# Performance work log

Measured on AMD Instinct MI355X. Metric: run time of the kernel, lower is better.

The kernel has to match this reference:

```python
import jax, jax.numpy as jnp
import numpy as np
from jax import lax

DIM, D_STATE, D_CONV, EXPAND = 96, 16, 4, 2
D_INNER = EXPAND * DIM          # 192
DT_RANK = (DIM + 15) // 16      # 6
B_, T_, H_, W_ = 2, 8, 32, 32   # L = T*H*W = 8192 tokens


def setup_inputs() -> dict:
    key = jax.random.key(0)
    ks = jax.random.split(key, 16)
    f = jnp.float32
    rn = lambda k, shape, s=0.02: jax.random.normal(k, shape, dtype=f) * s
    # S4D-real init for A_log, as in mamba_ssm
    A_init = jnp.log(jnp.tile(jnp.arange(1, D_STATE + 1, dtype=f), (D_INNER, 1)))
    return dict(
        x=jax.random.normal(ks[0], (B_, DIM, T_, H_, W_), dtype=f),
        ln_gamma=1.0 + rn(ks[1], (DIM,)),
        ln_beta=rn(ks[2], (DIM,)),
        in_proj_w=rn(ks[3], (2 * D_INNER, DIM)),
        conv_w=rn(ks[4], (D_INNER, 1, D_CONV), 0.1),
        conv_b=rn(ks[5], (D_INNER,)),
        x_proj_w=rn(ks[6], (DT_RANK + 2 * D_STATE, D_INNER)),
        dt_proj_w=rn(ks[7], (D_INNER, DT_RANK), 0.1),
        dt_proj_b=rn(ks[8], (D_INNER,)) + 0.5,
        A_log=A_init,
        D=jnp.ones((D_INNER,), f),
        conv_w_b=rn(ks[9], (D_INNER, 1, D_CONV), 0.1),
        conv_b_b=rn(ks[10], (D_INNER,)),
        x_proj_w_b=rn(ks[11], (DT_RANK + 2 * D_STATE, D_INNER)),
        dt_proj_w_b=rn(ks[12], (D_INNER, DT_RANK), 0.1),
        dt_proj_b_b=rn(ks[13], (D_INNER,)) + 0.5,
        A_log_b=A_init,
        D_b=jnp.ones((D_INNER,), f),
        out_proj_w=rn(ks[14], (DIM, D_INNER)),
    )


def serpentine(x):
    # continues_scan: reverse W on odd H rows so flattened (T,H,W) ordering is a
    # continuous path through the volume. Involutive => also rev_continues_scan.
    return x.at[..., 1::2, :].set(jnp.flip(x[..., 1::2, :], axis=-1))


def layer_norm(x, g, b, eps=1e-5):
    mu = jnp.mean(x, -1, keepdims=True)
    var = jnp.var(x, -1, keepdims=True)
    return (x - mu) * lax.rsqrt(var + eps) * g + b


def mamba_dir(x_in, z, conv_w, conv_b, x_proj_w, dt_proj_w, dt_proj_b, A_log, D):
    # x_in, z: (B, L, d_inner). One directional selective-scan branch.
    xc = lax.conv_general_dilated(
        x_in.swapaxes(1, 2), conv_w, (1,), [(D_CONV - 1, 0)],
        feature_group_count=D_INNER, dimension_numbers=('NCH', 'OIH', 'NCH'))
    xc = jax.nn.silu(xc + conv_b[None, :, None]).swapaxes(1, 2)  # (B,L,d_inner)
    dbl = jnp.einsum('bld,ed->ble', xc, x_proj_w)                # (B,L,dt_rank+2N)
    dt = jax.nn.softplus(
        jnp.einsum('blr,dr->bld', dbl[..., :DT_RANK], dt_proj_w) + dt_proj_b)
    Bm = dbl[..., DT_RANK:DT_RANK + D_STATE]                     # (B,L,N)
    Cm = dbl[..., DT_RANK + D_STATE:]                            # (B,L,N)
    A = -jnp.exp(A_log)                                          # (d_inner,N)

    def step(h, inp):
        dt_t, x_t, B_t, C_t = inp                                # (B,d),(B,d),(B,N),(B,N)
        h = jnp.exp(dt_t[..., None] * A) * h + (dt_t * x_t)[..., None] * B_t[:, None, :]
        return h, jnp.einsum('bdn,bn->bd', h, C_t)

    h0 = jnp.zeros((x_in.shape[0], D_INNER, D_STATE), x_in.dtype)
    xs = (dt.swapaxes(0, 1), xc.swapaxes(0, 1), Bm.swapaxes(0, 1), Cm.swapaxes(0, 1))
    _, ys = lax.scan(step, h0, xs)                               # (L,B,d_inner)
    y = ys.swapaxes(0, 1) + D * xc
    return y * jax.nn.silu(z)


def reference(x, ln_gamma, ln_beta, in_proj_w, conv_w, conv_b, x_proj_w,
              dt_proj_w, dt_proj_b, A_log, D, conv_w_b, conv_b_b, x_proj_w_b,
              dt_proj_w_b, dt_proj_b_b, A_log_b, D_b, out_proj_w):
    B, C, T, H, W = x.shape
    xs = serpentine(x)
    x_flat = xs.reshape(B, C, T * H * W).swapaxes(1, 2)          # (B,L,dim)
    xn = layer_norm(x_flat, ln_gamma, ln_beta)
    xz = jnp.einsum('bld,ed->ble', xn, in_proj_w)                # (B,L,2*d_inner)
    x_in, z = jnp.split(xz, 2, axis=-1)
    y_f = mamba_dir(x_in, z, conv_w, conv_b, x_proj_w, dt_proj_w,
                    dt_proj_b, A_log, D)
    y_b = jnp.flip(
        mamba_dir(jnp.flip(x_in, 1), jnp.flip(z, 1), conv_w_b, conv_b_b,
                  x_proj_w_b, dt_proj_w_b, dt_proj_b_b, A_log_b, D_b), 1)
    out = jnp.einsum('bld,ed->ble', y_f + y_b, out_proj_w)       # (B,L,dim)
    out = out.swapaxes(1, 2).reshape(B, C, T, H, W)
    return serpentine(out)
```

## Files before the change

### kernel.cpp

```cpp
#include <hip/hip_runtime.h>
#include <math.h>

#define LSEQ 8192
#define TS   32
#define NST  8

template<int CTRL>
__device__ __forceinline__ float dpp_add(float x) {
  const int y = __builtin_amdgcn_update_dpp(0, __float_as_int(x), CTRL, 0xF, 0xF, true);
  return x + __int_as_float(y);
}
__device__ __forceinline__ float red16(float x) {
  x = dpp_add<0xB1>(x);
  x = dpp_add<0x4E>(x);
  x = dpp_add<0x128>(x);
  x = dpp_add<0x124>(x);
  return x;
}

__global__ __launch_bounds__(256) void k0_wt(const float* __restrict__ xw_f,
    const float* __restrict__ xw_b, const float* __restrict__ in_w,
    const float* __restrict__ ow, float* __restrict__ xwT,
    float* __restrict__ inwT, float* __restrict__ owT) {
  const int step = gridDim.x * 256;
  const int t0 = blockIdx.x * 256 + threadIdx.x;
  for (int idx = t0; idx < 2 * 192 * 40; idx += step) {
    const int dir = idx / (192 * 40), rem = idx - dir * 192 * 40;
    const int k = rem / 40, r = rem - k * 40;
    const float* w = dir ? xw_b : xw_f;
    xwT[idx] = (r < 38) ? w[r * 192 + k] : 0.f;
  }
  for (int idx = t0; idx < 96 * 384; idx += step) {
    const int k = idx / 384, e = idx - k * 384;
    inwT[idx] = in_w[e * 96 + k];
  }
  for (int idx = t0; idx < 192 * 96; idx += step) {
    const int k = idx / 96, e = idx - k * 96;
    owT[idx] = ow[e * 192 + k];
  }
}

__global__ __launch_bounds__(256) void k1_serp_ln(const float* __restrict__ x,
    const float* __restrict__ gam, const float* __restrict__ bet,
    float* __restrict__ xnT) {
  const int b  = blockIdx.x >> 7;
  const int l0 = (blockIdx.x & 127) << 6;
  __shared__ float xs[96][65];
  __shared__ float mu[64], rs[64];
  const int tid = threadIdx.x;
  for (int idx = tid; idx < 96 * 64; idx += 256) {
    const int c = idx >> 6, l = idx & 63;
    const int lg = l0 + l;
    const int hh = (lg >> 5) & 31, w = lg & 31;
    const int lsrc = (hh & 1) ? (lg + 31 - 2 * w) : lg;
    xs[c][l] = x[(b * 96 + c) * LSEQ + lsrc];
  }
  __syncthreads();
  {
    const int l = tid >> 2, k = tid & 3;
    float s = 0.f, s2 = 0.f;
    for (int c = k; c < 96; c += 4) { const float v = xs[c][l]; s += v; s2 += v * v; }
    s  += __shfl_xor(s, 1);  s  += __shfl_xor(s, 2);
    s2 += __shfl_xor(s2, 1); s2 += __shfl_xor(s2, 2);
    if (k == 0) {
      const float m = s * (1.f / 96.f);
      const float var = s2 * (1.f / 96.f) - m * m;
      mu[l] = m; rs[l] = rsqrtf(var + 1e-5f);
    }
  }
  __syncthreads();
  for (int idx = tid; idx < 96 * 64; idx += 256) {
    const int c = idx >> 6, l = idx & 63;
    xnT[c * 16384 + (b << 13) + l0 + l] =
        (xs[c][l] - mu[l]) * rs[l] * gam[c] + bet[c];
  }
}

__global__ __launch_bounds__(256) void k2_inproj(const float* __restrict__ xnT,
    const float* __restrict__ inwT, float* __restrict__ xz) {
  const int m0 = blockIdx.x << 6;
  const int e0 = blockIdx.y << 6;
  __shared__ float As[96][67];
  __shared__ float Ws[96][67];
  const int tid = threadIdx.x;
  for (int idx = tid; idx < 96 * 64; idx += 256) {
    const int k = idx >> 6, r = idx & 63;
    As[k][r] = xnT[(size_t)k * 16384 + m0 + r];
    Ws[k][r] = inwT[k * 384 + e0 + r];
  }
  __syncthreads();
  const int tx = tid & 15, ty = tid >> 4;
  const int la = tx << 2, ea = ty << 2;
  float acc[4][4] = {};
  for (int k = 0; k < 96; ++k) {
    float av[4], bv[4];
#pragma unroll
    for (int i = 0; i < 4; ++i) av[i] = As[k][la + i];
#pragma unroll
    for (int j = 0; j < 4; ++j) bv[j] = Ws[k][ea + j];
#pragma unroll
    for (int j = 0; j < 4; ++j)
#pragma unroll
      for (int i = 0; i < 4; ++i) acc[j][i] = fmaf(bv[j], av[i], acc[j][i]);
  }
  const int b = m0 >> 13, l0 = m0 & (LSEQ - 1);
  const bool dos = (e0 >= 192);
#pragma unroll
  for (int j = 0; j < 4; ++j) {
    const int e = e0 + ea + j;
    float4 v;
    v.x = acc[j][0]; v.y = acc[j][1]; v.z = acc[j][2]; v.w = acc[j][3];
    if (dos) {
      v.x = v.x / (1.f + __expf(-v.x)); v.y = v.y / (1.f + __expf(-v.y));
      v.z = v.z / (1.f + __expf(-v.z)); v.w = v.w / (1.f + __expf(-v.w));
    }
    *(float4*)(&xz[((size_t)b * 384 + e) * LSEQ + l0 + la]) = v;
  }
}

__global__ __launch_bounds__(256) void k3a_conv(const float* __restrict__ xz,
    const float* __restrict__ cw_f, const float* __restrict__ cb_f,
    const float* __restrict__ cw_b, const float* __restrict__ cb_b,
    float* __restrict__ xc) {
  const int l = (blockIdx.x << 8) + threadIdx.x;
  const int d = blockIdx.y, b = blockIdx.z;
  const float* xin = xz + ((size_t)b * 384 + d) * LSEQ;
  float xv[7];
#pragma unroll
  for (int j = -3; j <= 3; ++j) {
    const int ls = l + j;
    xv[j + 3] = ((unsigned)ls < LSEQ) ? xin[ls] : 0.f;
  }
  float af = cb_f[d], ab = cb_b[d];
#pragma unroll
  for (int j = 0; j < 4; ++j) {
    af = fmaf(cw_f[d * 4 + j], xv[j], af);
    ab = fmaf(cw_b[d * 4 + j], xv[6 - j], ab);
  }
  xc[((size_t)(b)       * 192 + d) * LSEQ + l] = af / (1.f + __expf(-af));
  xc[((size_t)(2 + b)   * 192 + d) * LSEQ + l] = ab / (1.f + __expf(-ab));
}

__global__ __launch_bounds__(256, 2) void k3b_xproj(const float* __restrict__ xc,
    const float* __restrict__ xwT,
    const float* __restrict__ dtw_f, const float* __restrict__ dtb_f,
    const float* __restrict__ dtw_b, const float* __restrict__ dtb_b,
    float* __restrict__ dt, float* __restrict__ Bo, float* __restrict__ Co) {
  __shared__ float part[4][38][65];
  __shared__ float sdbl[6][65];
  const int dirb = blockIdx.y, dir = dirb >> 1;
  const int tid = threadIdx.x;
  const int lane = tid & 63, w = tid >> 6;
  const int l0 = blockIdx.x << 6;
  const float* pc = xc + (size_t)dirb * 192 * LSEQ + l0 + lane;
  const float* wt = xwT + dir * 192 * 40;
  float acc[38];
#pragma unroll
  for (int r = 0; r < 38; ++r) acc[r] = 0.f;
  const int kbase = w * 48;
#pragma unroll 2
  for (int kk = 0; kk < 48; ++kk) {
    const int k = kbase + kk;
    const float v = pc[(size_t)k * LSEQ];
    const float* wk = wt + k * 40;
#pragma unroll
    for (int r = 0; r < 38; ++r) acc[r] = fmaf(wk[r], v, acc[r]);
  }
#pragma unroll
  for (int r = 0; r < 38; ++r) part[w][r][lane] = acc[r];
  __syncthreads();
  {
    const int lq = tid >> 2, g = tid & 3;
    float vB[4], vC[4];
#pragma unroll
    for (int i = 0; i < 4; ++i) {
      const int rB = 6 + 4 * g + i, rC = 22 + 4 * g + i;
      float sB = 0.f, sC = 0.f;
#pragma unroll
      for (int ww = 0; ww < 4; ++ww) {
        sB += part[ww][rB][lq];
        sC += part[ww][rC][lq];
      }
      vB[i] = sB; vC[i] = sC;
    }
    const size_t off = ((size_t)dirb * LSEQ + l0 + lq) * 16 + 4 * g;
    *(float4*)&Bo[off] = make_float4(vB[0], vB[1], vB[2], vB[3]);
    *(float4*)&Co[off] = make_float4(vC[0], vC[1], vC[2], vC[3]);
  }
  for (int r = w; r < 6; r += 4) {
    float s = 0.f;
#pragma unroll
    for (int ww = 0; ww < 4; ++ww) s += part[ww][r][lane];
    sdbl[r][lane] = s;
  }
  __syncthreads();
  const float* dw = dir ? dtw_b : dtw_f;
  const float* db = dir ? dtb_b : dtb_f;
  const float v0 = sdbl[0][lane], v1 = sdbl[1][lane], v2 = sdbl[2][lane],
              v3 = sdbl[3][lane], v4 = sdbl[4][lane], v5 = sdbl[5][lane];
  float* pdt = dt + (size_t)dirb * 192 * LSEQ + l0 + lane;
#pragma unroll 2
  for (int i = 0; i < 48; ++i) {
    const int d = w * 48 + i;
    float s = db[d];
    s = fmaf(dw[d * 6 + 0], v0, s);
    s = fmaf(dw[d * 6 + 1], v1, s);
    s = fmaf(dw[d * 6 + 2], v2, s);
    s = fmaf(dw[d * 6 + 3], v3, s);
    s = fmaf(dw[d * 6 + 4], v4, s);
    s = fmaf(dw[d * 6 + 5], v5, s);
    pdt[(size_t)d * LSEQ] = (s > 20.f) ? s : __logf(1.f + __expf(s));
  }
}

template<int DIR>
__device__ __forceinline__ void scanA_body(
    float2 (*sdt)[16][34], float (*sb)[TS][16],
    const float* __restrict__ dtg, const float* __restrict__ xcg,
    const float* __restrict__ pB, const float* __restrict__ Al,
    float* __restrict__ Pb, float* __restrict__ Hb, int b, int c, int dg) {
  const int tid = threadIdx.x;
  const int dl = tid >> 4, n = tid & 15;
  const int dirb = DIR * 2 + b;
  const int d = (dg << 4) + dl;
  const float Adn = -__expf(Al[d * 16 + n]);
  const float* dtp = dtg + ((size_t)(dirb * 192) + d) * LSEQ;
  const float* xcp = xcg + ((size_t)(dirb * 192) + d) * LSEQ;
  const int c0 = c << 8;
  const int tl2 = (tid & 15) * 2;
  const int br = tid >> 3, bcc = (tid & 7) * 2;
  {
    const int t0 = c0 + (DIR ? (NST - 1) : 0) * TS;
    const float2 a  = *(const float2*)&dtp[t0 + tl2];
    const float2 xu = *(const float2*)&xcp[t0 + tl2];
    const float2 rb = *(const float2*)&pB[(size_t)(t0 + br) * 16 + bcc];
    float4 pk; pk.x = a.x; pk.y = a.x * xu.x; pk.z = a.y; pk.w = a.y * xu.y;
    *(float4*)&sdt[0][dl][tl2] = pk;
    *(float2*)&sb[0][br][bcc] = rb;
  }
  __syncthreads();
  float h = 0.f, dts = 0.f;
  int buf = 0;
  for (int i = 0; i < NST; ++i) {
    const int s = DIR ? (NST - 1 - i) : i;
    float2 a = make_float2(0.f, 0.f), xu = make_float2(0.f, 0.f);
    float2 rb = make_float2(0.f, 0.f);
    if (i + 1 < NST) {
      const int t0n = c0 + (DIR ? (s - 1) : (s + 1)) * TS;
      a   = *(const float2*)&dtp[t0n + tl2];
      xu  = *(const float2*)&xcp[t0n + tl2];
      rb  = *(const float2*)&pB[(size_t)(t0n + br) * 16 + bcc];
    }
#pragma unroll
    for (int tt = 0; tt < TS; ++tt) {
      const int t = DIR ? (TS - 1 - tt) : tt;
      const float2 xv = sdt[buf][dl][t];
      const float Bn = sb[buf][t][n];
      const float av = __expf(xv.x * Adn);
      h = fmaf(av, h, xv.y * Bn);
      dts += xv.x;
    }
    if (i + 1 < NST) {
      float4 pk; pk.x = a.x; pk.y = a.x * xu.x; pk.z = a.y; pk.w = a.y * xu.y;
      *(float4*)&sdt[buf ^ 1][dl][tl2] = pk;
      *(float2*)&sb[buf ^ 1][br][bcc] = rb;
    }
    __syncthreads();
    buf ^= 1;
  }
  const int o = ((dirb * 32 + c) * 192 + d) * 16 + n;
  Pb[o] = __expf(dts * Adn);
  Hb[o] = h;
}

__global__ __launch_bounds__(256) void k4_scanA(const float* __restrict__ dtg,
    const float* __restrict__ xcg, const float* __restrict__ Bo,
    const float* __restrict__ Al_f, const float* __restrict__ Al_b,
    float* __restrict__ Pb, float* __restrict__ Hb) {
  __shared__ float2 sdt[2][16][34];
  __shared__ float sb[2][TS][16];
  const int b = blockIdx.y, c = blockIdx.x & 31, dg = blockIdx.x >> 5;
  const float* pB0 = Bo + (size_t)(0 * 2 + b) * LSEQ * 16;
  const float* pB1 = Bo + (size_t)(1 * 2 + b) * LSEQ * 16;
  if (blockIdx.z == 0) scanA_body<0>(sdt, sb, dtg, xcg, pB0, Al_f, Pb, Hb, b, c, dg);
  else                 scanA_body<1>(sdt, sb, dtg, xcg, pB1, Al_b, Pb, Hb, b, c, dg);
}

__global__ __launch_bounds__(256) void k5_scanB(const float* __restrict__ Pb,
    const float* __restrict__ Hb, float* __restrict__ H0) {
  const int g = blockIdx.x * 256 + threadIdx.x;
  const int dirb = g / 3072, dn = g - dirb * 3072;
  const int dir = dirb >> 1;
  const int base = dirb * (32 * 3072) + dn;
  float h = 0.f;
  if (dir == 0) {
    for (int c = 0; c < 32; ++c) {
      const int o = base + c * 3072;
      H0[o] = h;
      h = fmaf(Pb[o], h, Hb[o]);
    }
  } else {
    for (int c = 31; c >= 0; --c) {
      const int o = base + c * 3072;
      H0[o] = h;
      h = fmaf(Pb[o], h, Hb[o]);
    }
  }
}

template<int DIR>
__device__ __forceinline__ void scanC_body(
    float2 (*sdt)[16][34], float2 (*sbc)[TS][16],
    const float* __restrict__ dtg, const float* __restrict__ xcg,
    const float* __restrict__ pB, const float* __restrict__ pC,
    const float* __restrict__ xz,
    const float* __restrict__ Al, const float* __restrict__ Dv_,
    const float* __restrict__ H0, float* __restrict__ yout,
    int b, int c, int dg) {
  const int tid = threadIdx.x;
  const int dl = tid >> 4, n = tid & 15;
  const int dirb = DIR * 2 + b;
  const int d = (dg << 4) + dl;
  const float Adn = -__expf(Al[d * 16 + n]);
  const float Dv = Dv_[d];
  const float* dtp = dtg + ((size_t)(dirb * 192) + d) * LSEQ;
  const float* xcp = xcg + ((size_t)(dirb * 192) + d) * LSEQ;
  const float* psp = xz + ((size_t)(b * 384) + 192 + d) * LSEQ;
  float* py = yout + ((size_t)(b * 192) + d) * LSEQ;
  const int o = ((dirb * 32 + c) * 192 + d) * 16 + n;
  const int c0 = c << 8;
  const int tl2 = (tid & 15) * 2;
  const int br = tid >> 3, bcc = (tid & 7) * 2;
  float h = H0[o];
  const int t00 = c0 + (DIR ? (NST - 1) : 0) * TS;
  {
    const float2 a  = *(const float2*)&dtp[t00 + tl2];
    const float2 xu = *(const float2*)&xcp[t00 + tl2];
    const float2 b2 = *(const float2*)&pB[(size_t)(t00 + br) * 16 + bcc];
    const float2 c2 = *(const float2*)&pC[(size_t)(t00 + br) * 16 + bcc];
    float4 pk; pk.x = a.x; pk.y = a.x * xu.x; pk.z = a.y; pk.w = a.y * xu.y;
    *(float4*)&sdt[0][dl][tl2] = pk;
    *(float4*)&sbc[0][br][bcc] = make_float4(b2.x, c2.x, b2.y, c2.y);
  }
  float cxa = xcp[t00 + n], cxb = xcp[t00 + 16 + n];
  float cspa = psp[t00 + n], cspb = psp[t00 + 16 + n];
  __syncthreads();
  int buf = 0;
  for (int i = 0; i < NST; ++i) {
    const int s = DIR ? (NST - 1 - i) : i;
    const int t0 = c0 + s * TS;
    float2 a = make_float2(0.f, 0.f), xu = make_float2(0.f, 0.f);
    float2 b2 = make_float2(0.f, 0.f), c2 = make_float2(0.f, 0.f);
    float nxa = 0.f, nxb = 0.f, nspa = 0.f, nspb = 0.f;
    if (i + 1 < NST) {
      const int t0n = c0 + (DIR ? (s - 1) : (s + 1)) * TS;
      a   = *(const float2*)&dtp[t0n + tl2];
      xu  = *(const float2*)&xcp[t0n + tl2];
      b2  = *(const float2*)&pB[(size_t)(t0n + br) * 16 + bcc];
      c2  = *(const float2*)&pC[(size_t)(t0n + br) * 16 + bcc];
      nxa = xcp[t0n + n]; nxb = xcp[t0n + 16 + n];
      nspa = psp[t0n + n]; nspb = psp[t0n + 16 + n];
    }
    float p0 = 0.f, p1 = 0.f;
#pragma unroll
    for (int tt = 0; tt < TS; ++tt) {
      const int t = DIR ? (TS - 1 - tt) : tt;
      const float2 xv = sdt[buf][dl][t];
      const float2 v = sbc[buf][t][n];
      const float av = __expf(xv.x * Adn);
      h = fmaf(av, h, xv.y * v.x);
      float p = red16(h * v.y);
      if (t < 16) p0 = ((t & 15) == n) ? p : p0;
      else        p1 = ((t & 15) == n) ? p : p1;
    }
    py[t0 + n]      = fmaf(Dv, cxa, p0) * cspa;
    py[t0 + 16 + n] = fmaf(Dv, cxb, p1) * cspb;
    if (i + 1 < NST) {
      float4 pk; pk.x = a.x; pk.y = a.x * xu.x; pk.z = a.y; pk.w = a.y * xu.y;
      *(float4*)&sdt[buf ^ 1][dl][tl2] = pk;
      *(float4*)&sbc[buf ^ 1][br][bcc] = make_float4(b2.x, c2.x, b2.y, c2.y);
      cxa = nxa; cxb = nxb; cspa = nspa; cspb = nspb;
    }
    __syncthreads();
    buf ^= 1;
  }
}

__global__ __launch_bounds__(256) void k6_scanC(const float* __restrict__ dtg,
    const float* __restrict__ xcg, const float* __restrict__ Bo,
    const float* __restrict__ Co, const float* __restrict__ xz,
    const float* __restrict__ Al_f, const float* __restrict__ Al_b,
    const float* __restrict__ D_f, const float* __restrict__ D_b,
    const float* __restrict__ H0,
    float* __restrict__ yf, float* __restrict__ yb) {
  __shared__ float2 sdt[2][16][34];
  __shared__ float2 sbc[2][TS][16];
  const int b = blockIdx.y, c = blockIdx.x & 31, dg = blockIdx.x >> 5;
  const float* pB0 = Bo + (size_t)(0 * 2 + b) * LSEQ * 16;
  const float* pB1 = Bo + (size_t)(1 * 2 + b) * LSEQ * 16;
  const float* pC0 = Co + (size_t)(0 * 2 + b) * LSEQ * 16;
  const float* pC1 = Co + (size_t)(1 * 2 + b) * LSEQ * 16;
  if (blockIdx.z == 0)
    scanC_body<0>(sdt, sbc, dtg, xcg, pB0, pC0, xz, Al_f, D_f, H0, yf, b, c, dg);
  else
    scanC_body<1>(sdt, sbc, dtg, xcg, pB1, pC1, xz, Al_b, D_b, H0, yb, b, c, dg);
}

__global__ __launch_bounds__(256) void k7_outproj(const float* __restrict__ yf,
    const float* __restrict__ yb, const float* __restrict__ owT,
    float* __restrict__ out) {
  const int m0 = blockIdx.x << 6;
  const int e0 = blockIdx.y * 48;
  const int b = m0 >> 13, l0 = m0 & (LSEQ - 1);
  __shared__ float As[48][65];
  __shared__ float Ws[48][49];
  const int tid = threadIdx.x;
  const int tx = tid & 15, ty = tid >> 4;
  const int la = tx << 2, ea = ty * 3;
  float acc[3][4] = {};
  for (int kc = 0; kc < 192; kc += 48) {
    for (int idx = tid; idx < 48 * 64; idx += 256) {
      const int k = idx >> 6, l = idx & 63;
      const size_t off = ((size_t)b * 192 + kc + k) * LSEQ + l0 + l;
      As[k][l] = yf[off] + yb[off];
    }
    for (int idx = tid; idx < 48 * 48; idx += 256) {
      const int k = idx / 48, e = idx - k * 48;
      Ws[k][e] = owT[(kc + k) * 96 + e0 + e];
    }
    __syncthreads();
#pragma unroll 4
    for (int k = 0; k < 48; ++k) {
      const float a0 = As[k][la], a1 = As[k][la + 1],
                  a2 = As[k][la + 2], a3 = As[k][la + 3];
      const float w0 = Ws[k][ea], w1 = Ws[k][ea + 1], w2 = Ws[k][ea + 2];
      acc[0][0] = fmaf(w0, a0, acc[0][0]); acc[0][1] = fmaf(w0, a1, acc[0][1]);
      acc[0][2] = fmaf(w0, a2, acc[0][2]); acc[0][3] = fmaf(w0, a3, acc[0][3]);
      acc[1][0] = fmaf(w1, a0, acc[1][0]); acc[1][1] = fmaf(w1, a1, acc[1][1]);
      acc[1][2] = fmaf(w1, a2, acc[1][2]); acc[1][3] = fmaf(w1, a3, acc[1][3]);
      acc[2][0] = fmaf(w2, a0, acc[2][0]); acc[2][1] = fmaf(w2, a1, acc[2][1]);
      acc[2][2] = fmaf(w2, a2, acc[2][2]); acc[2][3] = fmaf(w2, a3, acc[2][3]);
    }
    __syncthreads();
  }
#pragma unroll
  for (int j = 0; j < 3; ++j) {
    const int e = e0 + ea + j;
#pragma unroll
    for (int i = 0; i < 4; ++i) {
      const int l = l0 + la + i;
      const int hh = (l >> 5) & 31, ww = l & 31;
      const int lp = (hh & 1) ? (l + 31 - 2 * ww) : l;
      out[((size_t)b * 96 + e) * LSEQ + lp] = acc[j][i];
    }
  }
}

extern "C" void kernel_launch(void* const* d_in, const int* in_sizes, int n_in,
                              void* d_out, int out_size, void* d_ws, size_t ws_size,
                              hipStream_t stream) {
  const float* x     = (const float*)d_in[0];
  const float* ln_g  = (const float*)d_in[1];
  const float* ln_b  = (const float*)d_in[2];
  const float* in_w  = (const float*)d_in[3];
  const float* cw_f  = (const float*)d_in[4];
  const float* cb_f  = (const float*)d_in[5];
  const float* xw_f  = (const float*)d_in[6];
  const float* dtw_f = (const float*)d_in[7];
  const float* dtb_f = (const float*)d_in[8];
  const float* Al_f  = (const float*)d_in[9];
  const float* D_f   = (const float*)d_in[10];
  const float* cw_b  = (const float*)d_in[11];
  const float* cb_b  = (const float*)d_in[12];
  const float* xw_b  = (const float*)d_in[13];
  const float* dtw_b = (const float*)d_in[14];
  const float* dtb_b = (const float*)d_in[15];
  const float* Al_b  = (const float*)d_in[16];
  const float* D_b   = (const float*)d_in[17];
  const float* ow    = (const float*)d_in[18];
  float* out = (float*)d_out;

  float* ws = (float*)d_ws;
  float* xnT  = ws; ws += (size_t)16384 * 96;
  float* xz   = ws; ws += (size_t)2 * 384 * LSEQ;
  float* xc   = ws; ws += (size_t)4 * 192 * LSEQ;
  float* dt   = ws; ws += (size_t)4 * 192 * LSEQ;
  float* Bo   = ws; ws += (size_t)4 * LSEQ * 16;
  float* Co   = ws; ws += (size_t)4 * LSEQ * 16;
  float* yf   = ws; ws += (size_t)2 * 192 * LSEQ;
  float* yb   = ws; ws += (size_t)2 * 192 * LSEQ;
  float* Pb   = ws; ws += (size_t)4 * 32 * 192 * 16;
  float* Hb   = ws; ws += (size_t)4 * 32 * 192 * 16;
  float* H0   = ws; ws += (size_t)4 * 32 * 192 * 16;
  float* xwT  = ws; ws += (size_t)2 * 192 * 40;
  float* inwT = ws; ws += (size_t)96 * 384;
  float* owT  = ws; ws += (size_t)192 * 96;

  k0_wt<<<dim3(64), dim3(256), 0, stream>>>(xw_f, xw_b, in_w, ow, xwT, inwT, owT);
  k1_serp_ln<<<dim3(256), dim3(256), 0, stream>>>(x, ln_g, ln_b, xnT);
  k2_inproj<<<dim3(256, 6), dim3(256), 0, stream>>>(xnT, inwT, xz);
  k3a_conv<<<dim3(32, 192, 2), dim3(256), 0, stream>>>(xz, cw_f, cb_f, cw_b, cb_b, xc);
  k3b_xproj<<<dim3(128, 4), dim3(256), 0, stream>>>(xc, xwT,
      dtw_f, dtb_f, dtw_b, dtb_b, dt, Bo, Co);
  k4_scanA<<<dim3(384, 2, 2), dim3(256), 0, stream>>>(dt, xc, Bo,
      Al_f, Al_b, Pb, Hb);
  k5_scanB<<<dim3(48), dim3(256), 0, stream>>>(Pb, Hb, H0);
  k6_scanC<<<dim3(384, 2, 2), dim3(256), 0, stream>>>(dt, xc, Bo, Co,
      xz, Al_f, Al_b, D_f, D_b, H0, yf, yb);
  k7_outproj<<<dim3(256, 2), dim3(256), 0, stream>>>(yf, yb, owT, out);
}
```

Measured before the change: 201.5 us.

## Give each scan thread two states and vectorize GEMM shared loads

```diff
diff --git a/kernel.cpp b/kernel.cpp
--- a/kernel.cpp
+++ b/kernel.cpp
@@ -10,11 +10,10 @@
   const int y = __builtin_amdgcn_update_dpp(0, __float_as_int(x), CTRL, 0xF, 0xF, true);
   return x + __int_as_float(y);
 }
-__device__ __forceinline__ float red16(float x) {
+__device__ __forceinline__ float red8(float x) {
   x = dpp_add<0xB1>(x);
   x = dpp_add<0x4E>(x);
-  x = dpp_add<0x128>(x);
-  x = dpp_add<0x124>(x);
+  x += __int_as_float(__builtin_amdgcn_ds_swizzle(__float_as_int(x), 0x101F));
   return x;
 }
 
@@ -80,8 +79,8 @@
     const float* __restrict__ inwT, float* __restrict__ xz) {
   const int m0 = blockIdx.x << 6;
   const int e0 = blockIdx.y << 6;
-  __shared__ float As[96][67];
-  __shared__ float Ws[96][67];
+  __shared__ float As[96][68];
+  __shared__ float Ws[96][68];
   const int tid = threadIdx.x;
   for (int idx = tid; idx < 96 * 64; idx += 256) {
     const int k = idx >> 6, r = idx & 63;
@@ -93,15 +92,16 @@
   const int la = tx << 2, ea = ty << 2;
   float acc[4][4] = {};
   for (int k = 0; k < 96; ++k) {
-    float av[4], bv[4];
-#pragma unroll
-    for (int i = 0; i < 4; ++i) av[i] = As[k][la + i];
-#pragma unroll
-    for (int j = 0; j < 4; ++j) bv[j] = Ws[k][ea + j];
-#pragma unroll
-    for (int j = 0; j < 4; ++j)
-#pragma unroll
-      for (int i = 0; i < 4; ++i) acc[j][i] = fmaf(bv[j], av[i], acc[j][i]);
+    const float4 av = *(const float4*)&As[k][la];
+    const float4 bv = *(const float4*)&Ws[k][ea];
+    acc[0][0] = fmaf(bv.x, av.x, acc[0][0]); acc[0][1] = fmaf(bv.x, av.y, acc[0][1]);
+    acc[0][2] = fmaf(bv.x, av.z, acc[0][2]); acc[0][3] = fmaf(bv.x, av.w, acc[0][3]);
+    acc[1][0] = fmaf(bv.y, av.x, acc[1][0]); acc[1][1] = fmaf(bv.y, av.y, acc[1][1]);
+    acc[1][2] = fmaf(bv.y, av.z, acc[1][2]); acc[1][3] = fmaf(bv.y, av.w, acc[1][3]);
+    acc[2][0] = fmaf(bv.z, av.x, acc[2][0]); acc[2][1] = fmaf(bv.z, av.y, acc[2][1]);
+    acc[2][2] = fmaf(bv.z, av.z, acc[2][2]); acc[2][3] = fmaf(bv.z, av.w, acc[2][3]);
+    acc[3][0] = fmaf(bv.w, av.x, acc[3][0]); acc[3][1] = fmaf(bv.w, av.y, acc[3][1]);
+    acc[3][2] = fmaf(bv.w, av.z, acc[3][2]); acc[3][3] = fmaf(bv.w, av.w, acc[3][3]);
   }
   const int b = m0 >> 13, l0 = m0 & (LSEQ - 1);
   const bool dos = (e0 >= 192);
@@ -215,69 +215,86 @@
 
 template<int DIR>
 __device__ __forceinline__ void scanA_body(
-    float2 (*sdt)[16][34], float (*sb)[TS][16],
+    float2 (*sdt)[32][34], float (*sb)[TS][16],
     const float* __restrict__ dtg, const float* __restrict__ xcg,
     const float* __restrict__ pB, const float* __restrict__ Al,
     float* __restrict__ Pb, float* __restrict__ Hb, int b, int c, int dg) {
   const int tid = threadIdx.x;
-  const int dl = tid >> 4, n = tid & 15;
+  const int dl = tid >> 3, n = tid & 7;
   const int dirb = DIR * 2 + b;
-  const int d = (dg << 4) + dl;
-  const float Adn = -__expf(Al[d * 16 + n]);
-  const float* dtp = dtg + ((size_t)(dirb * 192) + d) * LSEQ;
-  const float* xcp = xcg + ((size_t)(dirb * 192) + d) * LSEQ;
+  const int d = (dg << 5) + dl;
+  const float Adn1 = -__expf(Al[d * 16 + n]);
+  const float Adn2 = -__expf(Al[d * 16 + n + 8]);
+  const size_t rowbase = ((size_t)(dirb * 192) + (dg << 5)) * LSEQ;
+  const float* dtp = dtg + rowbase;
+  const float* xcp = xcg + rowbase;
   const int c0 = c << 8;
-  const int tl2 = (tid & 15) * 2;
-  const int br = tid >> 3, bcc = (tid & 7) * 2;
+  const int sr0 = tid >> 4, spr = (tid & 15) * 2, sr1 = sr0 + 16;
+  const int wt = tid >> 2, wf = (tid & 3) * 4;
   {
-    const int t0 = c0 + (DIR ? (NST - 1) : 0) * TS;
-    const float2 a  = *(const float2*)&dtp[t0 + tl2];
-    const float2 xu = *(const float2*)&xcp[t0 + tl2];
-    const float2 rb = *(const float2*)&pB[(size_t)(t0 + br) * 16 + bcc];
-    float4 pk; pk.x = a.x; pk.y = a.x * xu.x; pk.z = a.y; pk.w = a.y * xu.y;
-    *(float4*)&sdt[0][dl][tl2] = pk;
-    *(float2*)&sb[0][br][bcc] = rb;
-  }
-  __syncthreads();
-  float h = 0.f, dts = 0.f;
+    const int tc = c0 + (DIR ? (NST - 1) : 0) * TS;
+    const float2 a0 = *(const float2*)&dtp[(size_t)sr0 * LSEQ + tc + spr];
+    const float2 x0 = *(const float2*)&xcp[(size_t)sr0 * LSEQ + tc + spr];
+    const float2 a1 = *(const float2*)&dtp[(size_t)sr1 * LSEQ + tc + spr];
+    const float2 x1 = *(const float2*)&xcp[(size_t)sr1 * LSEQ + tc + spr];
+    float4 k0; k0.x = a0.x; k0.y = a0.x * x0.x; k0.z = a0.y; k0.w = a0.y * x0.y;
+    float4 k1; k1.x = a1.x; k1.y = a1.x * x1.x; k1.z = a1.y; k1.w = a1.y * x1.y;
+    *(float4*)&sdt[0][sr0][spr] = k0;
+    *(float4*)&sdt[0][sr1][spr] = k1;
+    if (tid < 128) {
+      const float4 bv = *(const float4*)&pB[(size_t)(tc + wt) * 16 + wf];
+      *(float4*)&sb[0][wt][wf] = bv;
+    }
+  }
+  __syncthreads();
+  float h1 = 0.f, h2 = 0.f, dts = 0.f;
   int buf = 0;
   for (int i = 0; i < NST; ++i) {
     const int s = DIR ? (NST - 1 - i) : i;
-    float2 a = make_float2(0.f, 0.f), xu = make_float2(0.f, 0.f);
-    float2 rb = make_float2(0.f, 0.f);
+    float2 a0 = make_float2(0.f, 0.f), x0 = a0, a1 = a0, x1 = a0;
+    float4 bv = make_float4(0.f, 0.f, 0.f, 0.f);
     if (i + 1 < NST) {
-      const int t0n = c0 + (DIR ? (s - 1) : (s + 1)) * TS;
-      a   = *(const float2*)&dtp[t0n + tl2];
-      xu  = *(const float2*)&xcp[t0n + tl2];
-      rb  = *(const float2*)&pB[(size_t)(t0n + br) * 16 + bcc];
+      const int tn = c0 + (DIR ? (s - 1) : (s + 1)) * TS;
+      a0 = *(const float2*)&dtp[(size_t)sr0 * LSEQ + tn + spr];
+      x0 = *(const float2*)&xcp[(size_t)sr0 * LSEQ + tn + spr];
+      a1 = *(const float2*)&dtp[(size_t)sr1 * LSEQ + tn + spr];
+      x1 = *(const float2*)&xcp[(size_t)sr1 * LSEQ + tn + spr];
+      if (tid < 128) bv = *(const float4*)&pB[(size_t)(tn + wt) * 16 + wf];
     }
 #pragma unroll
     for (int tt = 0; tt < TS; ++tt) {
       const int t = DIR ? (TS - 1 - tt) : tt;
       const float2 xv = sdt[buf][dl][t];
-      const float Bn = sb[buf][t][n];
-      const float av = __expf(xv.x * Adn);
-      h = fmaf(av, h, xv.y * Bn);
+      const float B1 = sb[buf][t][n];
+      const float B2 = sb[buf][t][n + 8];
+      const float e1 = __expf(xv.x * Adn1);
+      const float e2 = __expf(xv.x * Adn2);
+      h1 = fmaf(e1, h1, xv.y * B1);
+      h2 = fmaf(e2, h2, xv.y * B2);
       dts += xv.x;
     }
     if (i + 1 < NST) {
-      float4 pk; pk.x = a.x; pk.y = a.x * xu.x; pk.z = a.y; pk.w = a.y * xu.y;
-      *(float4*)&sdt[buf ^ 1][dl][tl2] = pk;
-      *(float2*)&sb[buf ^ 1][br][bcc] = rb;
+      float4 k0; k0.x = a0.x; k0.y = a0.x * x0.x; k0.z = a0.y; k0.w = a0.y * x0.y;
+      float4 k1; k1.x = a1.x; k1.y = a1.x * x1.x; k1.z = a1.y; k1.w = a1.y * x1.y;
+      *(float4*)&sdt[buf ^ 1][sr0][spr] = k0;
+      *(float4*)&sdt[buf ^ 1][sr1][spr] = k1;
+      if (tid < 128) *(float4*)&sb[buf ^ 1][wt][wf] = bv;
     }
     __syncthreads();
     buf ^= 1;
   }
   const int o = ((dirb * 32 + c) * 192 + d) * 16 + n;
-  Pb[o] = __expf(dts * Adn);
-  Hb[o] = h;
+  Pb[o]     = __expf(dts * Adn1);
+  Pb[o + 8] = __expf(dts * Adn2);
+  Hb[o]     = h1;
+  Hb[o + 8] = h2;
 }
 
 __global__ __launch_bounds__(256) void k4_scanA(const float* __restrict__ dtg,
     const float* __restrict__ xcg, const float* __restrict__ Bo,
     const float* __restrict__ Al_f, const float* __restrict__ Al_b,
     float* __restrict__ Pb, float* __restrict__ Hb) {
-  __shared__ float2 sdt[2][16][34];
+  __shared__ float2 sdt[2][32][34];
   __shared__ float sb[2][TS][16];
   const int b = blockIdx.y, c = blockIdx.x & 31, dg = blockIdx.x >> 5;
   const float* pB0 = Bo + (size_t)(0 * 2 + b) * LSEQ * 16;
@@ -310,7 +327,7 @@
 
 template<int DIR>
 __device__ __forceinline__ void scanC_body(
-    float2 (*sdt)[16][34], float2 (*sbc)[TS][16],
+    float2 (*sdt)[32][34], float2 (*sbc)[TS][16],
     const float* __restrict__ dtg, const float* __restrict__ xcg,
     const float* __restrict__ pB, const float* __restrict__ pC,
     const float* __restrict__ xz,
@@ -318,68 +335,94 @@
     const float* __restrict__ H0, float* __restrict__ yout,
     int b, int c, int dg) {
   const int tid = threadIdx.x;
-  const int dl = tid >> 4, n = tid & 15;
+  const int dl = tid >> 3, n = tid & 7;
   const int dirb = DIR * 2 + b;
-  const int d = (dg << 4) + dl;
-  const float Adn = -__expf(Al[d * 16 + n]);
+  const int d = (dg << 5) + dl;
+  const float Adn1 = -__expf(Al[d * 16 + n]);
+  const float Adn2 = -__expf(Al[d * 16 + n + 8]);
   const float Dv = Dv_[d];
-  const float* dtp = dtg + ((size_t)(dirb * 192) + d) * LSEQ;
-  const float* xcp = xcg + ((size_t)(dirb * 192) + d) * LSEQ;
+  const size_t rowbase = ((size_t)(dirb * 192) + (dg << 5)) * LSEQ;
+  const float* dtp = dtg + rowbase;
+  const float* xcp = xcg + rowbase;
+  const float* xcq = xcg + ((size_t)(dirb * 192) + d) * LSEQ;
   const float* psp = xz + ((size_t)(b * 384) + 192 + d) * LSEQ;
   float* py = yout + ((size_t)(b * 192) + d) * LSEQ;
   const int o = ((dirb * 32 + c) * 192 + d) * 16 + n;
+  float h1 = H0[o], h2 = H0[o + 8];
   const int c0 = c << 8;
-  const int tl2 = (tid & 15) * 2;
-  const int br = tid >> 3, bcc = (tid & 7) * 2;
-  float h = H0[o];
-  const int t00 = c0 + (DIR ? (NST - 1) : 0) * TS;
+  const int sr0 = tid >> 4, spr = (tid & 15) * 2, sr1 = sr0 + 16;
+  const int sbt = tid >> 3, sbp = (tid & 7) * 2;
+  float cx0, cx1, cx2, cx3, sp0, sp1, sp2, sp3;
   {
-    const float2 a  = *(const float2*)&dtp[t00 + tl2];
-    const float2 xu = *(const float2*)&xcp[t00 + tl2];
-    const float2 b2 = *(const float2*)&pB[(size_t)(t00 + br) * 16 + bcc];
-    const float2 c2 = *(const float2*)&pC[(size_t)(t00 + br) * 16 + bcc];
-    float4 pk; pk.x = a.x; pk.y = a.x * xu.x; pk.z = a.y; pk.w = a.y * xu.y;
-    *(float4*)&sdt[0][dl][tl2] = pk;
-    *(float4*)&sbc[0][br][bcc] = make_float4(b2.x, c2.x, b2.y, c2.y);
-  }
-  float cxa = xcp[t00 + n], cxb = xcp[t00 + 16 + n];
-  float cspa = psp[t00 + n], cspb = psp[t00 + 16 + n];
+    const int tc = c0 + (DIR ? (NST - 1) : 0) * TS;
+    const float2 a0 = *(const float2*)&dtp[(size_t)sr0 * LSEQ + tc + spr];
+    const float2 x0 = *(const float2*)&xcp[(size_t)sr0 * LSEQ + tc + spr];
+    const float2 a1 = *(const float2*)&dtp[(size_t)sr1 * LSEQ + tc + spr];
+    const float2 x1 = *(const float2*)&xcp[(size_t)sr1 * LSEQ + tc + spr];
+    const float2 b2 = *(const float2*)&pB[(size_t)(tc + sbt) * 16 + sbp];
+    const float2 c2 = *(const float2*)&pC[(size_t)(tc + sbt) * 16 + sbp];
+    float4 k0; k0.x = a0.x; k0.y = a0.x * x0.x; k0.z = a0.y; k0.w = a0.y * x0.y;
+    float4 k1; k1.x = a1.x; k1.y = a1.x * x1.x; k1.z = a1.y; k1.w = a1.y * x1.y;
+    *(float4*)&sdt[0][sr0][spr] = k0;
+    *(float4*)&sdt[0][sr1][spr] = k1;
+    *(float4*)&sbc[0][sbt][sbp] = make_float4(b2.x, c2.x, b2.y, c2.y);
+    cx0 = xcq[tc + n];      cx1 = xcq[tc + 8 + n];
+    cx2 = xcq[tc + 16 + n]; cx3 = xcq[tc + 24 + n];
+    sp0 = psp[tc + n];      sp1 = psp[tc + 8 + n];
+    sp2 = psp[tc + 16 + n]; sp3 = psp[tc + 24 + n];
+  }
   __syncthreads();
   int buf = 0;
   for (int i = 0; i < NST; ++i) {
     const int s = DIR ? (NST - 1 - i) : i;
     const int t0 = c0 + s * TS;
-    float2 a = make_float2(0.f, 0.f), xu = make_float2(0.f, 0.f);
-    float2 b2 = make_float2(0.f, 0.f), c2 = make_float2(0.f, 0.f);
-    float nxa = 0.f, nxb = 0.f, nspa = 0.f, nspb = 0.f;
+    float2 a0 = make_float2(0.f, 0.f), x0 = a0, a1 = a0, x1 = a0, b2 = a0, c2 = a0;
+    float nx0 = 0.f, nx1 = 0.f, nx2 = 0.f, nx3 = 0.f;
+    float ns0 = 0.f, ns1 = 0.f, ns2 = 0.f, ns3 = 0.f;
     if (i + 1 < NST) {
-      const int t0n = c0 + (DIR ? (s - 1) : (s + 1)) * TS;
-      a   = *(const float2*)&dtp[t0n + tl2];
-      xu  = *(const float2*)&xcp[t0n + tl2];
-      b2  = *(const float2*)&pB[(size_t)(t0n + br) * 16 + bcc];
-      c2  = *(const float2*)&pC[(size_t)(t0n + br) * 16 + bcc];
-      nxa = xcp[t0n + n]; nxb = xcp[t0n + 16 + n];
-      nspa = psp[t0n + n]; nspb = psp[t0n + 16 + n];
-    }
-    float p0 = 0.f, p1 = 0.f;
+      const int tn = c0 + (DIR ? (s - 1) : (s + 1)) * TS;
+      a0 = *(const float2*)&dtp[(size_t)sr0 * LSEQ + tn + spr];
+      x0 = *(const float2*)&xcp[(size_t)sr0 * LSEQ + tn + spr];
+      a1 = *(const float2*)&dtp[(size_t)sr1 * LSEQ + tn + spr];
+      x1 = *(const float2*)&xcp[(size_t)sr1 * LSEQ + tn + spr];
+      b2 = *(const float2*)&pB[(size_t)(tn + sbt) * 16 + sbp];
+      c2 = *(const float2*)&pC[(size_t)(tn + sbt) * 16 + sbp];
+      nx0 = xcq[tn + n];      nx1 = xcq[tn + 8 + n];
+      nx2 = xcq[tn + 16 + n]; nx3 = xcq[tn + 24 + n];
+      ns0 = psp[tn + n];      ns1 = psp[tn + 8 + n];
+      ns2 = psp[tn + 16 + n]; ns3 = psp[tn + 24 + n];
+    }
+    float pq0 = 0.f, pq1 = 0.f, pq2 = 0.f, pq3 = 0.f;
 #pragma unroll
     for (int tt = 0; tt < TS; ++tt) {
       const int t = DIR ? (TS - 1 - tt) : tt;
       const float2 xv = sdt[buf][dl][t];
-      const float2 v = sbc[buf][t][n];
-      const float av = __expf(xv.x * Adn);
-      h = fmaf(av, h, xv.y * v.x);
-      float p = red16(h * v.y);
-      if (t < 16) p0 = ((t & 15) == n) ? p : p0;
-      else        p1 = ((t & 15) == n) ? p : p1;
-    }
-    py[t0 + n]      = fmaf(Dv, cxa, p0) * cspa;
-    py[t0 + 16 + n] = fmaf(Dv, cxb, p1) * cspb;
+      const float2 v1 = sbc[buf][t][n];
+      const float2 v2 = sbc[buf][t][n + 8];
+      const float e1 = __expf(xv.x * Adn1);
+      const float e2 = __expf(xv.x * Adn2);
+      h1 = fmaf(e1, h1, xv.y * v1.x);
+      h2 = fmaf(e2, h2, xv.y * v2.x);
+      float p = fmaf(h2, v2.y, h1 * v1.y);
+      p = red8(p);
+      const bool m = ((t & 7) == n);
+      if ((t >> 3) == 0)      pq0 = m ? p : pq0;
+      else if ((t >> 3) == 1) pq1 = m ? p : pq1;
+      else if ((t >> 3) == 2) pq2 = m ? p : pq2;
+      else                    pq3 = m ? p : pq3;
+    }
+    py[t0 + n]      = fmaf(Dv, cx0, pq0) * sp0;
+    py[t0 + 8 + n]  = fmaf(Dv, cx1, pq1) * sp1;
+    py[t0 + 16 + n] = fmaf(Dv, cx2, pq2) * sp2;
+    py[t0 + 24 + n] = fmaf(Dv, cx3, pq3) * sp3;
     if (i + 1 < NST) {
-      float4 pk; pk.x = a.x; pk.y = a.x * xu.x; pk.z = a.y; pk.w = a.y * xu.y;
-      *(float4*)&sdt[buf ^ 1][dl][tl2] = pk;
-      *(float4*)&sbc[buf ^ 1][br][bcc] = make_float4(b2.x, c2.x, b2.y, c2.y);
-      cxa = nxa; cxb = nxb; cspa = nspa; cspb = nspb;
+      float4 k0; k0.x = a0.x; k0.y = a0.x * x0.x; k0.z = a0.y; k0.w = a0.y * x0.y;
+      float4 k1; k1.x = a1.x; k1.y = a1.x * x1.x; k1.z = a1.y; k1.w = a1.y * x1.y;
+      *(float4*)&sdt[buf ^ 1][sr0][spr] = k0;
+      *(float4*)&sdt[buf ^ 1][sr1][spr] = k1;
+      *(float4*)&sbc[buf ^ 1][sbt][sbp] = make_float4(b2.x, c2.x, b2.y, c2.y);
+      cx0 = nx0; cx1 = nx1; cx2 = nx2; cx3 = nx3;
+      sp0 = ns0; sp1 = ns1; sp2 = ns2; sp3 = ns3;
     }
     __syncthreads();
     buf ^= 1;
@@ -393,7 +436,7 @@
     const float* __restrict__ D_f, const float* __restrict__ D_b,
     const float* __restrict__ H0,
     float* __restrict__ yf, float* __restrict__ yb) {
-  __shared__ float2 sdt[2][16][34];
+  __shared__ float2 sdt[2][32][34];
   __shared__ float2 sbc[2][TS][16];
   const int b = blockIdx.y, c = blockIdx.x & 31, dg = blockIdx.x >> 5;
   const float* pB0 = Bo + (size_t)(0 * 2 + b) * LSEQ * 16;
@@ -412,7 +455,7 @@
   const int m0 = blockIdx.x << 6;
   const int e0 = blockIdx.y * 48;
   const int b = m0 >> 13, l0 = m0 & (LSEQ - 1);
-  __shared__ float As[48][65];
+  __shared__ float As[48][68];
   __shared__ float Ws[48][49];
   const int tid = threadIdx.x;
   const int tx = tid & 15, ty = tid >> 4;
@@ -431,15 +474,14 @@
     __syncthreads();
 #pragma unroll 4
     for (int k = 0; k < 48; ++k) {
-      const float a0 = As[k][la], a1 = As[k][la + 1],
-                  a2 = As[k][la + 2], a3 = As[k][la + 3];
+      const float4 a4 = *(const float4*)&As[k][la];
       const float w0 = Ws[k][ea], w1 = Ws[k][ea + 1], w2 = Ws[k][ea + 2];
-      acc[0][0] = fmaf(w0, a0, acc[0][0]); acc[0][1] = fmaf(w0, a1, acc[0][1]);
-      acc[0][2] = fmaf(w0, a2, acc[0][2]); acc[0][3] = fmaf(w0, a3, acc[0][3]);
-      acc[1][0] = fmaf(w1, a0, acc[1][0]); acc[1][1] = fmaf(w1, a1, acc[1][1]);
-      acc[1][2] = fmaf(w1, a2, acc[1][2]); acc[1][3] = fmaf(w1, a3, acc[1][3]);
-      acc[2][0] = fmaf(w2, a0, acc[2][0]); acc[2][1] = fmaf(w2, a1, acc[2][1]);
-      acc[2][2] = fmaf(w2, a2, acc[2][2]); acc[2][3] = fmaf(w2, a3, acc[2][3]);
+      acc[0][0] = fmaf(w0, a4.x, acc[0][0]); acc[0][1] = fmaf(w0, a4.y, acc[0][1]);
+      acc[0][2] = fmaf(w0, a4.z, acc[0][2]); acc[0][3] = fmaf(w0, a4.w, acc[0][3]);
+      acc[1][0] = fmaf(w1, a4.x, acc[1][0]); acc[1][1] = fmaf(w1, a4.y, acc[1][1]);
+      acc[1][2] = fmaf(w1, a4.z, acc[1][2]); acc[1][3] = fmaf(w1, a4.w, acc[1][3]);
+      acc[2][0] = fmaf(w2, a4.x, acc[2][0]); acc[2][1] = fmaf(w2, a4.y, acc[2][1]);
+      acc[2][2] = fmaf(w2, a4.z, acc[2][2]); acc[2][3] = fmaf(w2, a4.w, acc[2][3]);
     }
     __syncthreads();
   }
@@ -502,10 +544,10 @@
   k3a_conv<<<dim3(32, 192, 2), dim3(256), 0, stream>>>(xz, cw_f, cb_f, cw_b, cb_b, xc);
   k3b_xproj<<<dim3(128, 4), dim3(256), 0, stream>>>(xc, xwT,
       dtw_f, dtb_f, dtw_b, dtb_b, dt, Bo, Co);
-  k4_scanA<<<dim3(384, 2, 2), dim3(256), 0, stream>>>(dt, xc, Bo,
+  k4_scanA<<<dim3(192, 2, 2), dim3(256), 0, stream>>>(dt, xc, Bo,
       Al_f, Al_b, Pb, Hb);
   k5_scanB<<<dim3(48), dim3(256), 0, stream>>>(Pb, Hb, H0);
-  k6_scanC<<<dim3(384, 2, 2), dim3(256), 0, stream>>>(dt, xc, Bo, Co,
+  k6_scanC<<<dim3(192, 2, 2), dim3(256), 0, stream>>>(dt, xc, Bo, Co,
       xz, Al_f, Al_b, D_f, D_b, H0, yf, yb);
   k7_outproj<<<dim3(256, 2), dim3(256), 0, stream>>>(yf, yb, owT, out);
 }
```

After: 192.4 us. 4.5% less time.
